# Kernel optimization log

Measured on AMD Instinct MI355X. Metric: run time of the kernel, lower is better.

Reference implementation:

```python
import jax, jax.numpy as jnp
import numpy as np

B, N, C = 8, 4096, 512
H = 8
HD = C // H          # head_dim = 64
KS = 5               # dwc kernel size
FF = 3.0             # focusing factor


def setup_inputs() -> dict:
    key = jax.random.key(0)
    ks = jax.random.split(key, 8)
    s = 1.0 / np.sqrt(C)
    return {
        "x": jax.random.normal(ks[0], (B, N, C), dtype=jnp.float32),
        "Wq": jax.random.normal(ks[1], (C, C), dtype=jnp.float32) * s,
        "Wkv": jax.random.normal(ks[2], (C, 2 * C), dtype=jnp.float32) * s,
        "Wproj": jax.random.normal(ks[3], (C, C), dtype=jnp.float32) * s,
        "b_proj": jax.random.normal(ks[4], (C,), dtype=jnp.float32) * 0.01,
        "scale_param": jnp.zeros((1, 1, C), dtype=jnp.float32),  # nn.Parameter(zeros)
        "dwc_w": jax.random.normal(ks[5], (HD, 1, KS, KS), dtype=jnp.float32) * 0.1,
        "dwc_b": jax.random.normal(ks[6], (HD,), dtype=jnp.float32) * 0.01,
    }


def _focus(t):
    # power-focusing map: preserve L2 norm while sharpening via elementwise power
    n = jnp.linalg.norm(t, axis=-1, keepdims=True)
    tp = t ** FF
    return tp / jnp.linalg.norm(tp, axis=-1, keepdims=True) * n


def reference(x, Wq, Wkv, Wproj, b_proj, scale_param, dwc_w, dwc_b):
    b, n, cdim = x.shape
    q = jax.nn.relu(x @ Wq) + 1e-6                      # [B,N,C]
    kv = x @ Wkv
    k = jax.nn.relu(kv[..., :cdim]) + 1e-6              # [B,N,C]
    v = kv[..., cdim:]                                  # [B,N,C]
    scale = jax.nn.softplus(scale_param)
    q = _focus(q / scale)
    k = _focus(k / scale)

    def split_heads(t):  # b n (h c) -> (b h) n c
        return t.reshape(b, n, H, HD).transpose(0, 2, 1, 3).reshape(b * H, n, HD)

    q, k, v = split_heads(q), split_heads(k), split_heads(v)
    i = j = n; c = d = HD
    z = 1.0 / (jnp.einsum('bic,bc->bi', q, k.sum(axis=1)) + 1e-6)  # [(bh), n]
    if i * j * (c + d) > c * d * (i + j):
        # linear path: O(N*c*d)
        kvm = jnp.einsum('bjc,bjd->bcd', k, v)          # [(bh), c, d]
        out = jnp.einsum('bic,bcd,bi->bid', q, kvm, z)
    else:
        qk = jnp.einsum('bic,bjc->bij', q, k)
        out = jnp.einsum('bij,bjd,bi->bid', qk, v, z)

    num = int(n ** 0.5)  # 64; N must be a perfect square
    fm = q.reshape(b * H, num, num, HD).transpose(0, 3, 1, 2)  # b c w h
    fm = jax.lax.conv_general_dilated(
        fm, dwc_w, window_strides=(1, 1), padding='SAME',
        feature_group_count=HD,
        dimension_numbers=('NCHW', 'OIHW', 'NCHW')) + dwc_b[None, :, None, None]
    fm = fm.transpose(0, 2, 3, 1).reshape(b * H, n, HD)
    out = out + fm
    out = out.reshape(b, H, n, HD).transpose(0, 2, 1, 3).reshape(b, n, cdim)
    return out @ Wproj + b_proj
```

## Files before the change

### kernel.cpp

```cpp
#include <hip/hip_runtime.h>
#include <cstddef>
#include <cstdint>

#define B_ 8
#define N_ 4096
#define C_ 512
#define H_ 8
#define HD_ 64
#define BH_ 64

typedef short  bf16x8 __attribute__((ext_vector_type(8)));
typedef float  f32x4  __attribute__((ext_vector_type(4)));
typedef ushort u16x8  __attribute__((ext_vector_type(8)));
typedef ushort u16x4  __attribute__((ext_vector_type(4)));

__device__ __forceinline__ float softplusf(float p) {
  return (p > 20.f) ? p : log1pf(expf(p));
}

__device__ __forceinline__ ushort f2bf(float f) {
  union { float f; unsigned u; } c; c.f = f;
  const unsigned r = c.u + 0x7fffu + ((c.u >> 16) & 1u);
  return (ushort)(r >> 16);
}
__device__ __forceinline__ float bf2f(ushort h) {
  union { unsigned u; float f; } c; c.u = ((unsigned)h) << 16;
  return c.f;
}

#define GLOAD16(g, l)                                                        \
  __builtin_amdgcn_global_load_lds(                                          \
      (const __attribute__((address_space(1))) void*)(g),                    \
      (__attribute__((address_space(3))) void*)(l), 16, 0, 0)

__global__ void scale_kernel(const float* __restrict__ sp, float* __restrict__ sinv)
{
  const int c = threadIdx.x;
  sinv[c] = 1.f / softplusf(sp[c]);
}

__global__ __launch_bounds__(256) void cvt_hi(const float* __restrict__ in,
                                              ushort* __restrict__ hi)
{
  const size_t i = (size_t)blockIdx.x * 256 + threadIdx.x;
  const float4 a = ((const float4*)in)[i * 2];
  const float4 b = ((const float4*)in)[i * 2 + 1];
  const float f[8] = {a.x, a.y, a.z, a.w, b.x, b.y, b.z, b.w};
  u16x8 h;
  #pragma unroll
  for (int j = 0; j < 8; ++j) h[j] = f2bf(f[j]);
  *(u16x8*)&hi[i * 8] = h;
}

__global__ __launch_bounds__(256) void cvt_w_t(const float* __restrict__ in,
                                               ushort* __restrict__ hi, int Nn)
{
  const int t  = blockIdx.x * 256 + threadIdx.x;
  const int n  = t >> 6;
  const int k8 = (t & 63) * 8;
  u16x8 h;
  #pragma unroll
  for (int j = 0; j < 8; ++j) h[j] = f2bf(in[(size_t)(k8 + j) * Nn + n]);
  *(u16x8*)&hi[(size_t)n * 512 + k8] = h;
}

__global__ __launch_bounds__(512, 2) void gemm_bf16(
    const ushort* __restrict__ Ah, const ushort* __restrict__ Bh,
    const float* __restrict__ bias,
    ushort* __restrict__ ob0, ushort* __restrict__ ob1, ushort* __restrict__ ob2,
    float* __restrict__ outf,
    int ncolb, int s1, int s2, int r0, int r1, int r2)
{
  __shared__ ushort lds[2][16384];
  const int tid = threadIdx.x;
  const int bid = blockIdx.x;
  const int loc = bid >> 3;
  const int xcd = bid & 7;
  const int row0 = ((xcd << 4) + loc / ncolb) * 256;
  const int col0 = (loc % ncolb) * 256;

  const int lane = tid & 63;
  const int li   = lane & 15;
  const int kq   = lane >> 4;
  const int w    = tid >> 6;
  const int wr   = (w >> 2) * 128;
  const int wc   = (w & 3) * 64;
  const int wbase = tid & 448;

  f32x4 acc[8][4] = {};

  auto STAGE = [&](int buf, int t) {
    ushort* l = &lds[buf][0];
    const int k0 = t * 32;
    #pragma unroll
    for (int it = 0; it < 2; ++it) {
      const int c   = it * 512 + tid;
      const int cw  = it * 512 + wbase;
      const int kb  = c >> 8;
      const int row = c & 255;
      GLOAD16(Ah + (size_t)(row0 + row) * 512 + k0 + kb * 8, &l[cw * 8]);
    }
    #pragma unroll
    for (int it = 0; it < 2; ++it) {
      const int c   = it * 512 + tid;
      const int cw  = it * 512 + wbase;
      const int kb  = c >> 8;
      const int col = c & 255;
      GLOAD16(Bh + (size_t)(col0 + col) * 512 + k0 + kb * 8, &l[8192 + cw * 8]);
    }
  };

  auto COMPUTE = [&](int buf) {
    const ushort* l = &lds[buf][0];
    bf16x8 bv[4];
    #pragma unroll
    for (int n = 0; n < 4; ++n)
      bv[n] = *(const bf16x8*)&l[8192 + (kq * 256 + wc + n * 16 + li) * 8];
    __builtin_amdgcn_s_setprio(1);
    #pragma unroll
    for (int m = 0; m < 8; ++m) {
      const bf16x8 av = *(const bf16x8*)&l[(kq * 256 + wr + m * 16 + li) * 8];
      #pragma unroll
      for (int n = 0; n < 4; ++n)
        acc[m][n] = __builtin_amdgcn_mfma_f32_16x16x32_bf16(av, bv[n], acc[m][n], 0, 0, 0);
    }
    __builtin_amdgcn_s_setprio(0);
  };

  STAGE(0, 0);
  __syncthreads();
  #pragma unroll 1
  for (int t = 0; t < 7; ++t) {
    STAGE(1, 2 * t + 1);
    COMPUTE(0);
    __syncthreads();
    STAGE(0, 2 * t + 2);
    COMPUTE(1);
    __syncthreads();
  }
  STAGE(1, 15);
  COMPUTE(0);
  __syncthreads();
  COMPUTE(1);

  if (outf) {
    #pragma unroll
    for (int m = 0; m < 8; ++m)
      #pragma unroll
      for (int n = 0; n < 4; ++n) {
        const int col = col0 + wc + n * 16 + li;
        const int row = row0 + wr + m * 16 + kq * 4;
        const float bv = bias[col];
        #pragma unroll
        for (int r = 0; r < 4; ++r)
          outf[(size_t)(row + r) * 512 + col] = acc[m][n][r] + bv;
      }
  } else {
    ushort* dest; int cbase, relu;
    if (col0 < s1)      { dest = ob0; cbase = 0;  relu = r0; }
    else if (col0 < s2) { dest = ob1; cbase = s1; relu = r1; }
    else                { dest = ob2; cbase = s2; relu = r2; }
    #pragma unroll
    for (int m = 0; m < 8; ++m)
      #pragma unroll
      for (int n = 0; n < 4; ++n) {
        const int col = col0 + wc + n * 16 + li;
        const int row = row0 + wr + m * 16 + kq * 4;
        #pragma unroll
        for (int r = 0; r < 4; ++r) {
          float v = acc[m][n][r];
          if (relu) v = fmaxf(v, 0.f) + 1e-6f;
          dest[(size_t)(row + r) * 512 + (col - cbase)] = f2bf(v);
        }
      }
  }
}

__global__ __launch_bounds__(256) void focus2(ushort* __restrict__ qb, ushort* __restrict__ kb,
                                              const float* __restrict__ sinv)
{
  const int rid  = blockIdx.x * 4 + (threadIdx.x >> 6);
  const int lane = threadIdx.x & 63;
  ushort* t = (rid < B_ * N_) ? qb : kb;
  const int row = rid & (B_ * N_ - 1);
  ushort* p = t + (size_t)row * 512 + lane * 8;
  const u16x8 raw = *(const u16x8*)p;
  const float4 sa = *(const float4*)&sinv[lane * 8];
  const float4 sb = *(const float4*)&sinv[lane * 8 + 4];
  const float sc[8] = {sa.x, sa.y, sa.z, sa.w, sb.x, sb.y, sb.z, sb.w};
  float tv[8];
  float s2 = 0.f, s6 = 0.f;
  #pragma unroll
  for (int i = 0; i < 8; ++i) {
    const float x = bf2f(raw[i]) * sc[i];
    tv[i] = x;
    const float x3 = x * x * x;
    s2 = fmaf(x, x, s2);
    s6 = fmaf(x3, x3, s6);
  }
  #pragma unroll
  for (int off = 32; off > 0; off >>= 1) {
    s2 += __shfl_xor(s2, off);
    s6 += __shfl_xor(s6, off);
  }
  const float f = sqrtf(s2 / s6);
  u16x8 o;
  #pragma unroll
  for (int i = 0; i < 8; ++i) o[i] = f2bf(tv[i] * tv[i] * tv[i] * f);
  *(u16x8*)p = o;
}

__global__ __launch_bounds__(256, 2) void kvm_kernel(
    const ushort* __restrict__ kf, const ushort* __restrict__ vf,
    float* __restrict__ kvmT, float* __restrict__ ksum)
{
  __shared__ ushort KT[2048];
  __shared__ ushort VT[2048];
  const int bh = blockIdx.x, bb = bh >> 3, h = bh & 7;
  const int n0 = blockIdx.y * 512;
  const int tid = threadIdx.x;
  const int lane = tid & 63;
  const int li   = lane & 15;
  const int kq   = lane >> 4;
  const int w    = tid >> 6;
  const int r    = tid >> 3;
  const int cg   = (tid & 7) * 8;

  f32x4 acc[4] = {};
  float ks[8] = {};

  u16x8 kraw = *(const u16x8*)&kf[((size_t)(bb * N_ + n0 + r)) * 512 + h * 64 + cg];
  u16x8 vraw = *(const u16x8*)&vf[((size_t)(bb * N_ + n0 + r)) * 512 + h * 64 + cg];

  #pragma unroll 1
  for (int t = 0; t < 16; ++t) {
    u16x8 knext = kraw, vnext = vraw;
    if (t < 15) {
      const size_t gn = ((size_t)(bb * N_ + n0 + (t + 1) * 32 + r)) * 512 + h * 64 + cg;
      knext = *(const u16x8*)&kf[gn];
      vnext = *(const u16x8*)&vf[gn];
    }
    #pragma unroll
    for (int j = 0; j < 8; ++j) {
      const int c = cg + j;
      const int p = (r >> 3) ^ ((c ^ (c >> 3)) & 3);
      const int idx = c * 32 + p * 8 + (r & 7);
      KT[idx] = kraw[j];
      VT[idx] = vraw[j];
      ks[j] += bf2f(kraw[j]);
    }
    __syncthreads();
    {
      const int ca = w * 16 + li;
      const bf16x8 av = *(const bf16x8*)&KT[ca * 32 + ((kq ^ ((ca ^ (ca >> 3)) & 3)) * 8)];
      #pragma unroll
      for (int dt = 0; dt < 4; ++dt) {
        const int cb = dt * 16 + li;
        const bf16x8 bv = *(const bf16x8*)&VT[cb * 32 + ((kq ^ ((cb ^ (cb >> 3)) & 3)) * 8)];
        acc[dt] = __builtin_amdgcn_mfma_f32_16x16x32_bf16(av, bv, acc[dt], 0, 0, 0);
      }
    }
    __syncthreads();
    kraw = knext;
    vraw = vnext;
  }

  #pragma unroll
  for (int dt = 0; dt < 4; ++dt)
    #pragma unroll
    for (int rr = 0; rr < 4; ++rr)
      atomicAdd(&kvmT[(size_t)(bh * 64 + dt * 16 + li) * 64 + w * 16 + kq * 4 + rr],
                acc[dt][rr]);
  #pragma unroll
  for (int j = 0; j < 8; ++j) {
    float s = ks[j];
    s += __shfl_xor(s, 8);
    s += __shfl_xor(s, 16);
    s += __shfl_xor(s, 32);
    if ((lane & 56) == 0) atomicAdd(&ksum[bh * 64 + cg + j], s);
  }
}

__global__ __launch_bounds__(256, 3) void attnout_kernel(
    const ushort* __restrict__ qf, const float* __restrict__ kvmT,
    const float* __restrict__ ksum, ushort* __restrict__ out)
{
  __shared__ ushort As[8 * 256 * 8];
  __shared__ ushort Bs[8 * 64 * 8];
  __shared__ float zrow[256];
  __shared__ float ksl[64];
  const int bh = blockIdx.x, bb = bh >> 3, h = bh & 7;
  const int n0 = blockIdx.y * 256;
  const int tid = threadIdx.x;
  const int lane = tid & 63;
  const int li   = lane & 15;
  const int kq   = lane >> 4;
  const int wv   = tid >> 6;
  const int w64  = tid & 192;

  #pragma unroll
  for (int it = 0; it < 8; ++it) {
    const int c   = it * 256 + tid;
    const int cw  = it * 256 + w64;
    const int kb  = c >> 8;
    const int row = c & 255;
    GLOAD16(qf + ((size_t)(bb * N_ + n0 + row)) * 512 + h * 64 + kb * 8,
            &As[cw * 8]);
  }
  {
    const int d  = tid >> 2;
    const int cg = (tid & 3) * 16;
    const float* src = &kvmT[(size_t)(bh * 64 + d) * 64 + cg];
    const float4 f0 = *(const float4*)&src[0];
    const float4 f1 = *(const float4*)&src[4];
    const float4 f2 = *(const float4*)&src[8];
    const float4 f3 = *(const float4*)&src[12];
    u16x8 b0, b1;
    b0[0]=f2bf(f0.x); b0[1]=f2bf(f0.y); b0[2]=f2bf(f0.z); b0[3]=f2bf(f0.w);
    b0[4]=f2bf(f1.x); b0[5]=f2bf(f1.y); b0[6]=f2bf(f1.z); b0[7]=f2bf(f1.w);
    b1[0]=f2bf(f2.x); b1[1]=f2bf(f2.y); b1[2]=f2bf(f2.z); b1[3]=f2bf(f2.w);
    b1[4]=f2bf(f3.x); b1[5]=f2bf(f3.y); b1[6]=f2bf(f3.z); b1[7]=f2bf(f3.w);
    *(u16x8*)&Bs[(((cg >> 3)    ) * 64 + d) * 8] = b0;
    *(u16x8*)&Bs[(((cg >> 3) + 1) * 64 + d) * 8] = b1;
  }
  if (tid < 64) ksl[tid] = ksum[bh * 64 + tid];
  __syncthreads();

  {
    float p = 0.f;
    #pragma unroll
    for (int kb = 0; kb < 8; ++kb) {
      const u16x8 qv = *(const u16x8*)&As[(kb * 256 + tid) * 8];
      #pragma unroll
      for (int j = 0; j < 8; ++j) p = fmaf(bf2f(qv[j]), ksl[kb * 8 + j], p);
    }
    zrow[tid] = 1.f / (p + 1e-6f);
  }

  f32x4 acc2[4][4] = {};
  #pragma unroll
  for (int kh = 0; kh < 2; ++kh) {
    bf16x8 bv[4];
    #pragma unroll
    for (int dt = 0; dt < 4; ++dt)
      bv[dt] = *(const bf16x8*)&Bs[((kh * 4 + kq) * 64 + dt * 16 + li) * 8];
    #pragma unroll
    for (int mt = 0; mt < 4; ++mt) {
      const bf16x8 av = *(const bf16x8*)&As[((kh * 4 + kq) * 256 + wv * 64 + mt * 16 + li) * 8];
      #pragma unroll
      for (int dt = 0; dt < 4; ++dt)
        acc2[mt][dt] = __builtin_amdgcn_mfma_f32_16x16x32_bf16(av, bv[dt], acc2[mt][dt], 0, 0, 0);
    }
  }
  __syncthreads();

  #pragma unroll
  for (int mt = 0; mt < 4; ++mt) {
    const float4 zv = *(const float4*)&zrow[wv * 64 + mt * 16 + kq * 4];
    const float za[4] = {zv.x, zv.y, zv.z, zv.w};
    const int rowb = n0 + wv * 64 + mt * 16 + kq * 4;
    #pragma unroll
    for (int dt = 0; dt < 4; ++dt) {
      const int col = h * 64 + dt * 16 + li;
      #pragma unroll
      for (int r = 0; r < 4; ++r)
        out[((size_t)(bb * N_ + rowb + r)) * 512 + col] = f2bf(acc2[mt][dt][r] * za[r]);
    }
  }
}

__global__ __launch_bounds__(256) void dwconv_hi(
    const ushort* __restrict__ qf, const float* __restrict__ w,
    const float* __restrict__ wb, const ushort* __restrict__ ano,
    ushort* __restrict__ oh)
{
  __shared__ float ws_[64 * 25];
  const int tid = threadIdx.x;
  for (int i = tid; i < 64 * 25; i += 256) ws_[i] = w[i];
  __syncthreads();

  const int bh = blockIdx.x, bb = bh >> 3, h = bh & 7;
  const int hd = tid & 63;
  const int s  = blockIdx.y * 4 + (tid >> 6);
  const int x  = s & 63;
  const int y0 = (s >> 6) * 8;

  float wreg[25];
  #pragma unroll
  for (int i = 0; i < 25; ++i) wreg[i] = ws_[hd * 25 + i];

  float acc[8];
  const float bias = wb[hd];
  #pragma unroll
  for (int j = 0; j < 8; ++j) acc[j] = bias;

  const ushort* base = qf + (size_t)bb * N_ * 512 + h * 64 + hd;
  #pragma unroll
  for (int kx = 0; kx < 5; ++kx) {
    const int xx  = x + kx - 2;
    const bool xok = (unsigned)xx < 64u;
    const int xxc = min(max(xx, 0), 63);
    float col[12];
    #pragma unroll
    for (int r = 0; r < 12; ++r) {
      const int yy  = y0 + r - 2;
      const bool ok = xok && ((unsigned)yy < 64u);
      const int yyc = min(max(yy, 0), 63);
      const float v = bf2f(base[(size_t)(yyc * 64 + xxc) * 512]);
      col[r] = ok ? v : 0.f;
    }
    #pragma unroll
    for (int ky = 0; ky < 5; ++ky) {
      const float wv = wreg[ky * 5 + kx];
      #pragma unroll
      for (int j = 0; j < 8; ++j)
        acc[j] = fmaf(wv, col[j + ky], acc[j]);
    }
  }

  #pragma unroll
  for (int j = 0; j < 8; ++j) {
    const int p = (y0 + j) * 64 + x;
    const size_t idx = ((size_t)(bb * N_ + p)) * 512 + h * 64 + hd;
    oh[idx] = f2bf(bf2f(ano[idx]) + acc[j]);
  }
}

extern "C" void kernel_launch(void* const* d_in, const int* in_sizes, int n_in,
                              void* d_out, int out_size, void* d_ws, size_t ws_size,
                              hipStream_t stream) {
  (void)in_sizes; (void)n_in; (void)out_size; (void)ws_size;
  const float* x     = (const float*)d_in[0];
  const float* Wq    = (const float*)d_in[1];
  const float* Wkv   = (const float*)d_in[2];
  const float* Wp    = (const float*)d_in[3];
  const float* bp    = (const float*)d_in[4];
  const float* sp    = (const float*)d_in[5];
  const float* dwc_w = (const float*)d_in[6];
  const float* dwc_b = (const float*)d_in[7];
  float* out = (float*)d_out;

  char* ws = (char*)d_ws;
  ushort* xh   = (ushort*)ws;
  ushort* qbuf = (ushort*)(ws + 33554432ull);
  ushort* kbuf = (ushort*)(ws + 67108864ull);
  char*   w0   = ws + 100663296ull;
  ushort* Bqh  = (ushort*)w0;
  ushort* Bph  = Bqh + 786432;
  float*  kvmb = (float*)(Bph + 262144);
  float*  ksum = kvmb + 262144;
  float*  sinv = ksum + 4096;
  ushort* vbuf = (ushort*)d_out;
  ushort* ano  = kbuf;

  const int M = B_ * N_;

  scale_kernel<<<1, 512, 0, stream>>>(sp, sinv);
  cvt_hi<<<8192, 256, 0, stream>>>(x, xh);
  cvt_w_t<<<128, 256, 0, stream>>>(Wq, Bqh, 512);
  cvt_w_t<<<256, 256, 0, stream>>>(Wkv, Bqh + 262144, 1024);
  cvt_w_t<<<128, 256, 0, stream>>>(Wp, Bph, 512);
  gemm_bf16<<<768, 512, 0, stream>>>(
      xh, Bqh, nullptr, qbuf, kbuf, vbuf, nullptr, 6, 512, 1024, 1, 1, 0);
  focus2<<<2 * M / 4, 256, 0, stream>>>(qbuf, kbuf, sinv);
  hipMemsetAsync(kvmb, 0, (262144 + 4096) * sizeof(float), stream);
  kvm_kernel<<<dim3(BH_, 8), 256, 0, stream>>>(kbuf, vbuf, kvmb, ksum);
  attnout_kernel<<<dim3(BH_, N_ / 256), 256, 0, stream>>>(qbuf, kvmb, ksum, ano);
  dwconv_hi<<<dim3(BH_, 128), 256, 0, stream>>>(qbuf, dwc_w, dwc_b, ano, xh);
  gemm_bf16<<<256, 512, 0, stream>>>(
      xh, Bph, bp, nullptr, nullptr, nullptr, out, 2, 512, 512, 0, 0, 0);
}
```

Measured before the change: 288.1 us.

## Stage q tile with halo in LDS for depthwise conv

The depthwise 5x5 conv kernel now stages a 12-row by 64-column halo tile of q for one head into shared memory using 16-byte loads, and each thread computes an 8x8 output patch from LDS. Previously every thread read 60 scattered bf16 values straight from global memory. The goal is to cut redundant global traffic and uncoalesced 2-byte loads. In exchange the grid shrinks to 512 blocks of 512 threads using 96KB of LDS each, which lowers occupancy, and the inner loop over x is kept rolled.

```diff
diff --git a/kernel.cpp b/kernel.cpp
--- a/kernel.cpp
+++ b/kernel.cpp
@@ -369,60 +369,69 @@
   }
 }
 
-__global__ __launch_bounds__(256) void dwconv_hi(
+__global__ __launch_bounds__(512, 1) void dwconv_hi(
     const ushort* __restrict__ qf, const float* __restrict__ w,
     const float* __restrict__ wb, const ushort* __restrict__ ano,
     ushort* __restrict__ oh)
 {
-  __shared__ float ws_[64 * 25];
+  __shared__ ushort qs[12 * 64 * 64];
   const int tid = threadIdx.x;
-  for (int i = tid; i < 64 * 25; i += 256) ws_[i] = w[i];
+  const int bh = blockIdx.x, bb = bh >> 3, h = bh & 7;
+  const int y0 = blockIdx.y * 8;
+
+  #pragma unroll
+  for (int it = 0; it < 12; ++it) {
+    const int idx = it * 512 + tid;
+    const int pix = idx >> 3;
+    const int seg = idx & 7;
+    const int row = pix >> 6;
+    const int x   = pix & 63;
+    const int yy  = min(max(y0 - 2 + row, 0), 63);
+    GLOAD16(qf + ((size_t)(bb * N_ + yy * 64 + x)) * 512 + h * 64 + seg * 8,
+            &qs[idx * 8]);
+  }
   __syncthreads();
 
-  const int bh = blockIdx.x, bb = bh >> 3, h = bh & 7;
   const int hd = tid & 63;
-  const int s  = blockIdx.y * 4 + (tid >> 6);
-  const int x  = s & 63;
-  const int y0 = (s >> 6) * 8;
-
+  const int xg = tid >> 6;
   float wreg[25];
   #pragma unroll
-  for (int i = 0; i < 25; ++i) wreg[i] = ws_[hd * 25 + i];
-
-  float acc[8];
+  for (int i = 0; i < 25; ++i) wreg[i] = w[hd * 25 + i];
   const float bias = wb[hd];
-  #pragma unroll
-  for (int j = 0; j < 8; ++j) acc[j] = bias;
-
-  const ushort* base = qf + (size_t)bb * N_ * 512 + h * 64 + hd;
-  #pragma unroll
-  for (int kx = 0; kx < 5; ++kx) {
-    const int xx  = x + kx - 2;
-    const bool xok = (unsigned)xx < 64u;
-    const int xxc = min(max(xx, 0), 63);
-    float col[12];
-    #pragma unroll
-    for (int r = 0; r < 12; ++r) {
-      const int yy  = y0 + r - 2;
-      const bool ok = xok && ((unsigned)yy < 64u);
-      const int yyc = min(max(yy, 0), 63);
-      const float v = bf2f(base[(size_t)(yyc * 64 + xxc) * 512]);
-      col[r] = ok ? v : 0.f;
-    }
-    #pragma unroll
-    for (int ky = 0; ky < 5; ++ky) {
-      const float wv = wreg[ky * 5 + kx];
-      #pragma unroll
-      for (int j = 0; j < 8; ++j)
-        acc[j] = fmaf(wv, col[j + ky], acc[j]);
-    }
-  }
-
-  #pragma unroll
+
+  #pragma unroll 1
   for (int j = 0; j < 8; ++j) {
-    const int p = (y0 + j) * 64 + x;
-    const size_t idx = ((size_t)(bb * N_ + p)) * 512 + h * 64 + hd;
-    oh[idx] = f2bf(bf2f(ano[idx]) + acc[j]);
+    const int x = xg * 8 + j;
+    float acc[8];
+    #pragma unroll
+    for (int yy = 0; yy < 8; ++yy) acc[yy] = bias;
+    #pragma unroll
+    for (int kx = 0; kx < 5; ++kx) {
+      const int xx  = x + kx - 2;
+      const bool xok = (unsigned)xx < 64u;
+      const int xxc = min(max(xx, 0), 63);
+      float col[12];
+      #pragma unroll
+      for (int r = 0; r < 12; ++r) {
+        const int yy = y0 + r - 2;
+        const bool ok = xok && ((unsigned)yy < 64u);
+        const float v = bf2f(qs[(r * 64 + xxc) * 64 + hd]);
+        col[r] = ok ? v : 0.f;
+      }
+      #pragma unroll
+      for (int ky = 0; ky < 5; ++ky) {
+        const float wv = wreg[ky * 5 + kx];
+        #pragma unroll
+        for (int yy = 0; yy < 8; ++yy)
+          acc[yy] = fmaf(wv, col[yy + ky], acc[yy]);
+      }
+    }
+    #pragma unroll
+    for (int yy = 0; yy < 8; ++yy) {
+      const int p = (y0 + yy) * 64 + x;
+      const size_t idx = ((size_t)(bb * N_ + p)) * 512 + h * 64 + hd;
+      oh[idx] = f2bf(bf2f(ano[idx]) + acc[yy]);
+    }
   }
 }
 
@@ -466,7 +475,7 @@
   hipMemsetAsync(kvmb, 0, (262144 + 4096) * sizeof(float), stream);
   kvm_kernel<<<dim3(BH_, 8), 256, 0, stream>>>(kbuf, vbuf, kvmb, ksum);
   attnout_kernel<<<dim3(BH_, N_ / 256), 256, 0, stream>>>(qbuf, kvmb, ksum, ano);
-  dwconv_hi<<<dim3(BH_, 128), 256, 0, stream>>>(qbuf, dwc_w, dwc_b, ano, xh);
+  dwconv_hi<<<dim3(BH_, 8), 512, 0, stream>>>(qbuf, dwc_w, dwc_b, ano, xh);
   gemm_bf16<<<256, 512, 0, stream>>>(
       xh, Bph, bp, nullptr, nullptr, nullptr, out, 2, 512, 512, 0, 0, 0);
 }
```

After: 289.1 us. About the same (+0.4%).
